# Performance work log

Measured on AMD Instinct MI355X. Metric: run time of the kernel, lower is better.

Reference implementation:

```python
import jax, jax.numpy as jnp
import numpy as np

N_NODES = 50000
N_EDGES = 800000
NUM_FEATS = 512
NUM_CLASSES = 64
NUM_LAYERS = 4


def setup_inputs() -> dict:
    key = jax.random.key(0)
    k1, k2, k3 = jax.random.split(key, 3)
    x = jax.random.normal(k1, (N_NODES, NUM_FEATS), dtype=jnp.float32)
    # glorot init for weight [num_feats, num_classes]
    scale = jnp.sqrt(6.0 / (NUM_FEATS + NUM_CLASSES)).astype(jnp.float32)
    weight = jax.random.uniform(k2, (NUM_FEATS, NUM_CLASSES), dtype=jnp.float32,
                                minval=-scale, maxval=scale)
    edge_index = jax.random.randint(k3, (2, N_EDGES), 0, N_NODES, dtype=jnp.int64)
    return {"x": x, "weight": weight, "edge_index": edge_index}


def reference(x, weight, edge_index):
    row, col = edge_index[0], edge_index[1]  # [E], [E]
    # symmetric GCN normalization: deg^{-1/2}[row] * deg^{-1/2}[col]
    deg = jax.ops.segment_sum(jnp.ones((edge_index.shape[1],), dtype=x.dtype),
                              row, num_segments=x.shape[0])  # [N]
    deg_inv_sqrt = jnp.where(deg > 0, jax.lax.rsqrt(jnp.maximum(deg, 1e-12)), 0.0)
    norm = (deg_inv_sqrt[row] * deg_inv_sqrt[col])[:, None]  # [E, 1]

    h = x @ weight  # [N, num_classes] (dropout skipped: eval mode)
    for _ in range(NUM_LAYERS):
        # gather source features, scale by edge norm, scatter-add to destinations
        msg = norm * h[row]  # [E, num_classes]
        h = jax.ops.segment_sum(msg, col, num_segments=x.shape[0])  # [N, num_classes]
        # type_norm == 'None' -> layers_bn is identity
    return h
```

## Files before the change

### kernel.cpp

```cpp
#include <hip/hip_runtime.h>
#include <hip/hip_fp16.h>

#define NFEAT 512
#define NCLS  64
#define NNODES 50000
#define NW    (NNODES / 4)
#define NB    256
#define NG    8
#define SLOTS 64

typedef unsigned int uint;
using short8 = __attribute__((ext_vector_type(8))) short;
using f32x4  = __attribute__((ext_vector_type(4))) float;

static __device__ __forceinline__ unsigned short f32_to_bf16_rne(float f) {
    unsigned u = __float_as_uint(f);
    unsigned r = u + 0x7FFFu + ((u >> 16) & 1u);
    return (unsigned short)(r >> 16);
}
static __device__ __forceinline__ float bf16_to_f32(unsigned short b) {
    return __uint_as_float(((unsigned)b) << 16);
}
static __device__ __forceinline__ uint cvt_pk_bf16(float a, float b) {
    uint r;
    asm("v_cvt_pk_bf16_f32 %0, %1, %2" : "=v"(r) : "v"(a), "v"(b));
    return r;
}
static __device__ __forceinline__ void split_bf16x8(const float* xs, short8& ahi, short8& alo) {
    union { uint u[4]; short8 s; } H, L;
#pragma unroll
    for (int t = 0; t < 4; ++t) {
        float x0 = xs[2 * t], x1 = xs[2 * t + 1];
        uint hp = cvt_pk_bf16(x0, x1);
        float f0 = __uint_as_float(hp << 16);
        float f1 = __uint_as_float(hp & 0xffff0000u);
        uint lp = cvt_pk_bf16(x0 - f0, x1 - f1);
        H.u[t] = hp; L.u[t] = lp;
    }
    ahi = H.s; alo = L.s;
}


__global__ __launch_bounds__(256) void hist_packw_kernel(
        const int* __restrict__ row, const int* __restrict__ col,
        const float* __restrict__ w,
        uint* __restrict__ degB, uint* __restrict__ cntB,
        short8* __restrict__ wp, int E, int CH) {
    __shared__ __align__(16) uint h[2 * NW];
    int b = blockIdx.x;
    if (b < NB) {
        for (int i = threadIdx.x; i < 2 * NW; i += 256) h[i] = 0;
        __syncthreads();
        int e0 = b * CH, e1 = min(E, e0 + CH);
        for (int e = e0 + threadIdx.x; e < e1; e += 256) {
            int c = col[e], r = row[e];
            atomicAdd(&h[c >> 2], 1u << ((c & 3) * 8));
            atomicAdd(&h[NW + (r >> 2)], 1u << ((r & 3) * 8));
        }
        __syncthreads();
        uint4* cb = reinterpret_cast<uint4*>(cntB + (size_t)b * NW);
        uint4* db = reinterpret_cast<uint4*>(degB + (size_t)b * NW);
        const uint4* c4 = reinterpret_cast<const uint4*>(h);
        const uint4* d4 = reinterpret_cast<const uint4*>(h + NW);
        for (int i = threadIdx.x; i < NW / 4; i += 256) cb[i] = c4[i];
        for (int i = threadIdx.x; i < NW / 4; i += 256) db[i] = d4[i];
        return;
    }
    int gid = (b - NB) * 256 + threadIdx.x;
    int lane = gid & 63;
    int F = gid >> 6;
    int s = F & 1;
    int nt = (F >> 1) & 3;
    int kk = F >> 3;
    int k0 = kk * 32 + (lane >> 4) * 8;
    int c  = nt * 16 + (lane & 15);
    short8 v;
#pragma unroll
    for (int j = 0; j < 8; ++j) {
        float xv = w[(k0 + j) * NCLS + c];
        unsigned short hi = f32_to_bf16_rne(xv);
        unsigned short outv = hi;
        if (s) outv = f32_to_bf16_rne(xv - bf16_to_f32(hi));
        v[j] = (short)outv;
    }
    wp[gid] = v;
}


__global__ __launch_bounds__(256) void scan_sub_kernel(uint* __restrict__ cntB,
                                                       const uint* __restrict__ degB,
                                                       uint* __restrict__ cntSub,
                                                       uint* __restrict__ degSub) {
    int gid = blockIdx.x * 256 + threadIdx.x;
    if (gid >= 2 * NG * NW) return;
    int half = gid / (NG * NW);
    int rem  = gid % (NG * NW);
    int g = rem / NW, wi = rem % NW;
    if (half == 0) {
        uint run = 0;
#pragma unroll 8
        for (int b = g * 32; b < g * 32 + 32; ++b) {
            uint v = cntB[(size_t)b * NW + wi];
            cntB[(size_t)b * NW + wi] = run;
            run += v;
        }
        cntSub[(size_t)g * NW + wi] = run;
    } else {
        uint run = 0;
#pragma unroll 8
        for (int b = g * 32; b < g * 32 + 32; ++b) run += degB[(size_t)b * NW + wi];
        degSub[(size_t)g * NW + wi] = run;
    }
}


__global__ __launch_bounds__(256) void scan_top_kernel(uint* __restrict__ cntSub,
                                                       const uint* __restrict__ degSub,
                                                       int* __restrict__ cntTot,
                                                       float* __restrict__ dinv) {
    int wi = blockIdx.x * 256 + threadIdx.x;
    if (wi >= NW) return;
    uint run = 0;
#pragma unroll
    for (int g = 0; g < NG; ++g) {
        uint v = cntSub[(size_t)g * NW + wi];
        cntSub[(size_t)g * NW + wi] = run;
        run += v;
    }
    int4 t = { (int)(run & 255), (int)((run >> 8) & 255),
               (int)((run >> 16) & 255), (int)(run >> 24) };
    *reinterpret_cast<int4*>(cntTot + wi * 4) = t;

    uint run2 = 0;
#pragma unroll
    for (int g = 0; g < NG; ++g) run2 += degSub[(size_t)g * NW + wi];
    int d0 = run2 & 255, d1 = (run2 >> 8) & 255, d2 = (run2 >> 16) & 255, d3 = run2 >> 24;
    float4 dv;
    dv.x = d0 ? rsqrtf((float)d0) : 0.0f;
    dv.y = d1 ? rsqrtf((float)d1) : 0.0f;
    dv.z = d2 ? rsqrtf((float)d2) : 0.0f;
    dv.w = d3 ? rsqrtf((float)d3) : 0.0f;
    *reinterpret_cast<float4*>(dinv + wi * 4) = dv;
}


__global__ __launch_bounds__(256, 2) void place_matmul_kernel(
        const int* __restrict__ row, const int* __restrict__ col,
        const uint* __restrict__ offB, const uint* __restrict__ cntSub,
        int* __restrict__ slots,
        const float* __restrict__ x, const short8* __restrict__ wp,
        const float* __restrict__ dinv, __half* __restrict__ u0,
        int N, int E, int CH) {
    __shared__ __align__(16) uint sh[NW];
    int b = blockIdx.x;

    if (b < NB) {
        uint4* c4 = reinterpret_cast<uint4*>(sh);
        const uint4* o4 = reinterpret_cast<const uint4*>(offB + (size_t)b * NW);
        const uint4* s4 = reinterpret_cast<const uint4*>(cntSub + (size_t)(b >> 5) * NW);
        for (int i = threadIdx.x; i < NW / 4; i += 256) {
            uint4 a = o4[i], d = s4[i];
            a.x += d.x; a.y += d.y; a.z += d.z; a.w += d.w;
            c4[i] = a;
        }
        __syncthreads();
        int e0 = b * CH, e1 = min(E, e0 + CH);
        for (int e = e0 + threadIdx.x; e < e1; e += 256) {
            int c = col[e];
            uint old = atomicAdd(&sh[c >> 2], 1u << ((c & 3) * 8));
            int pos = (old >> ((c & 3) * 8)) & 255;
            if (pos < SLOTS) slots[(c << 6) + pos] = row[e];
        }
        return;
    }

    int tile = b - NB;
    int tid = threadIdx.x;
    int wave = tid >> 6, lane = tid & 63;
    int rlo = lane & 15, khi = lane >> 4;
    int row0 = tile * 128 + wave * 32;

    size_t roff[2];
#pragma unroll
    for (int rg = 0; rg < 2; ++rg) {
        int rr = row0 + rg * 16 + rlo;
        if (rr > N - 1) rr = N - 1;
        roff[rg] = (size_t)rr * NFEAT + khi * 8;
    }

    f32x4 acc[2][4];
#pragma unroll
    for (int rg = 0; rg < 2; ++rg)
#pragma unroll
        for (int nt = 0; nt < 4; ++nt) acc[rg][nt] = f32x4{0.f, 0.f, 0.f, 0.f};

    const short8* fbase = wp + lane;
    for (int ch = 0; ch < 4; ++ch) {
#pragma unroll
        for (int kk = 0; kk < 4; ++kk) {
            const short8* fb = fbase + ch * 2048 + kk * 512;
            short8 bh0 = fb[0],   bl0 = fb[64];
            short8 bh1 = fb[128], bl1 = fb[192];
            short8 bh2 = fb[256], bl2 = fb[320];
            short8 bh3 = fb[384], bl3 = fb[448];
            int kg = ch * 128 + kk * 32;
#pragma unroll
            for (int rg = 0; rg < 2; ++rg) {
                float4 xa = *reinterpret_cast<const float4*>(x + roff[rg] + kg);
                float4 xb = *reinterpret_cast<const float4*>(x + roff[rg] + kg + 4);
                float xs[8] = {xa.x, xa.y, xa.z, xa.w, xb.x, xb.y, xb.z, xb.w};
                short8 ahi, alo;
                split_bf16x8(xs, ahi, alo);
                acc[rg][0] = __builtin_amdgcn_mfma_f32_16x16x32_bf16(ahi, bh0, acc[rg][0], 0, 0, 0);
                acc[rg][1] = __builtin_amdgcn_mfma_f32_16x16x32_bf16(ahi, bh1, acc[rg][1], 0, 0, 0);
                acc[rg][2] = __builtin_amdgcn_mfma_f32_16x16x32_bf16(ahi, bh2, acc[rg][2], 0, 0, 0);
                acc[rg][3] = __builtin_amdgcn_mfma_f32_16x16x32_bf16(ahi, bh3, acc[rg][3], 0, 0, 0);
                acc[rg][0] = __builtin_amdgcn_mfma_f32_16x16x32_bf16(alo, bh0, acc[rg][0], 0, 0, 0);
                acc[rg][1] = __builtin_amdgcn_mfma_f32_16x16x32_bf16(alo, bh1, acc[rg][1], 0, 0, 0);
                acc[rg][2] = __builtin_amdgcn_mfma_f32_16x16x32_bf16(alo, bh2, acc[rg][2], 0, 0, 0);
                acc[rg][3] = __builtin_amdgcn_mfma_f32_16x16x32_bf16(alo, bh3, acc[rg][3], 0, 0, 0);
                acc[rg][0] = __builtin_amdgcn_mfma_f32_16x16x32_bf16(ahi, bl0, acc[rg][0], 0, 0, 0);
                acc[rg][1] = __builtin_amdgcn_mfma_f32_16x16x32_bf16(ahi, bl1, acc[rg][1], 0, 0, 0);
                acc[rg][2] = __builtin_amdgcn_mfma_f32_16x16x32_bf16(ahi, bl2, acc[rg][2], 0, 0, 0);
                acc[rg][3] = __builtin_amdgcn_mfma_f32_16x16x32_bf16(ahi, bl3, acc[rg][3], 0, 0, 0);
            }
        }
    }

#pragma unroll
    for (int rg = 0; rg < 2; ++rg) {
        int rbase = row0 + rg * 16 + khi * 4;
#pragma unroll
        for (int j = 0; j < 4; ++j) {
            int r = rbase + j;
            if (r < N) {
                float dn = dinv[r];
                __half* op = u0 + ((size_t)r << 6) + rlo;
                op[0]  = __float2half(acc[rg][0][j] * dn);
                op[16] = __float2half(acc[rg][1][j] * dn);
                op[32] = __float2half(acc[rg][2][j] * dn);
                op[48] = __float2half(acc[rg][3][j] * dn);
            }
        }
    }
}


__global__ __launch_bounds__(256) void gather_kernel(const __half* __restrict__ u,
                                                     const int* __restrict__ cntTot,
                                                     int* __restrict__ slots,
                                                     const float* __restrict__ dinv,
                                                     __half* __restrict__ out_h,
                                                     float* __restrict__ out_f,
                                                     int N, int sq, int dosort) {
    int wid = blockIdx.x * 4 + (threadIdx.x >> 6);
    if (wid >= N) return;
    int lane = threadIdx.x & 63;
    int q = lane >> 3;
    int p = lane & 7;
    int cq = cntTot[wid];
    cq = (cq < SLOTS) ? cq : SLOTS;
    int* sl = slots + (wid << 6);
    int s_l = sl[lane];

    if (dosort) {
        int v = (lane < cq) ? s_l : 0x7fffffff;
#pragma unroll
        for (int k = 2; k <= 64; k <<= 1) {
#pragma unroll
            for (int j = k >> 1; j >= 1; j >>= 1) {
                int pv = __shfl_xor(v, j);
                int lo = min(v, pv), hi = max(v, pv);
                bool up = ((lane & k) == 0);
                v = (((lane & j) == 0) == up) ? lo : hi;
            }
        }
        s_l = v;
        if (lane < cq) sl[lane] = v;
    }

    float a0=0.f,a1=0.f,a2=0.f,a3=0.f,a4=0.f,a5=0.f,a6=0.f,a7=0.f;
    float b0=0.f,b1=0.f,b2=0.f,b3=0.f,b4=0.f,b5=0.f,b6=0.f,b7=0.f;
#pragma unroll
    for (int j = 0; j < 8; j += 2) {
        int i0 = q + 8 * j;
        int i1 = q + 8 * (j + 1);
        int s0 = __shfl(s_l, i0);
        int s1 = __shfl(s_l, i1);
        if (i0 < cq) {
            uint4 d0 = *reinterpret_cast<const uint4*>(u + ((size_t)s0 << 6) + p * 8);
            float2 f0 = __half22float2(*reinterpret_cast<__half2*>(&d0.x));
            float2 f1 = __half22float2(*reinterpret_cast<__half2*>(&d0.y));
            float2 f2 = __half22float2(*reinterpret_cast<__half2*>(&d0.z));
            float2 f3 = __half22float2(*reinterpret_cast<__half2*>(&d0.w));
            a0 += f0.x; a1 += f0.y; a2 += f1.x; a3 += f1.y;
            a4 += f2.x; a5 += f2.y; a6 += f3.x; a7 += f3.y;
        }
        if (i1 < cq) {
            uint4 d1 = *reinterpret_cast<const uint4*>(u + ((size_t)s1 << 6) + p * 8);
            float2 g0 = __half22float2(*reinterpret_cast<__half2*>(&d1.x));
            float2 g1 = __half22float2(*reinterpret_cast<__half2*>(&d1.y));
            float2 g2 = __half22float2(*reinterpret_cast<__half2*>(&d1.z));
            float2 g3 = __half22float2(*reinterpret_cast<__half2*>(&d1.w));
            b0 += g0.x; b1 += g0.y; b2 += g1.x; b3 += g1.y;
            b4 += g2.x; b5 += g2.y; b6 += g3.x; b7 += g3.y;
        }
    }
    a0 += b0; a1 += b1; a2 += b2; a3 += b3;
    a4 += b4; a5 += b5; a6 += b6; a7 += b7;
#pragma unroll
    for (int off = 8; off < 64; off <<= 1) {
        a0 += __shfl_xor(a0, off); a1 += __shfl_xor(a1, off);
        a2 += __shfl_xor(a2, off); a3 += __shfl_xor(a3, off);
        a4 += __shfl_xor(a4, off); a5 += __shfl_xor(a5, off);
        a6 += __shfl_xor(a6, off); a7 += __shfl_xor(a7, off);
    }
    if (q == 0) {
        float sc = dinv[wid];
        if (sq) {
            sc *= sc;
            __half2 h0 = __floats2half2_rn(a0 * sc, a1 * sc);
            __half2 h1 = __floats2half2_rn(a2 * sc, a3 * sc);
            __half2 h2 = __floats2half2_rn(a4 * sc, a5 * sc);
            __half2 h3 = __floats2half2_rn(a6 * sc, a7 * sc);
            uint4 d;
            d.x = *reinterpret_cast<uint*>(&h0);
            d.y = *reinterpret_cast<uint*>(&h1);
            d.z = *reinterpret_cast<uint*>(&h2);
            d.w = *reinterpret_cast<uint*>(&h3);
            *reinterpret_cast<uint4*>(out_h + ((size_t)wid << 6) + p * 8) = d;
        } else {
            float4 r0 = {a0 * sc, a1 * sc, a2 * sc, a3 * sc};
            float4 r1 = {a4 * sc, a5 * sc, a6 * sc, a7 * sc};
            float4* op = reinterpret_cast<float4*>(out_f + ((size_t)wid << 6) + p * 8);
            op[0] = r0;
            op[1] = r1;
        }
    }
}


extern "C" void kernel_launch(void* const* d_in, const int* in_sizes, int n_in,
                              void* d_out, int out_size, void* d_ws, size_t ws_size,
                              hipStream_t stream) {
    const float* x = (const float*)d_in[0];
    const float* w = (const float*)d_in[1];
    const int*   ei = (const int*)d_in[2];

    int N = in_sizes[0] / NFEAT;
    int E = in_sizes[2] / 2;
    const int* row = ei;
    const int* col = ei + E;
    float* out = (float*)d_out;

    auto align256 = [](size_t v) { return (v + 255) & ~(size_t)255; };
    char* ws = (char*)d_ws;
    size_t off = 0;
    uint* cntB   = (uint*)(ws + off);   off += align256((size_t)NB * NW * sizeof(uint));
    uint* degB   = (uint*)(ws + off);   off += align256((size_t)NB * NW * sizeof(uint));
    uint* cntSub = (uint*)(ws + off);   off += align256((size_t)NG * NW * sizeof(uint));
    uint* degSub = (uint*)(ws + off);   off += align256((size_t)NG * NW * sizeof(uint));
    int* cntTot  = (int*)(ws + off);    off += align256((size_t)NNODES * sizeof(int));
    float* dinv  = (float*)(ws + off);  off += align256((size_t)NNODES * sizeof(float));
    short8* wp   = (short8*)(ws + off); off += align256((size_t)8192 * sizeof(short8));
    int* slots   = (int*)(ws + off);    off += align256((size_t)NNODES * SLOTS * sizeof(int));
    __half* uA   = (__half*)(ws + off); off += align256((size_t)NNODES * NCLS * sizeof(__half));
    __half* uB   = (__half*)(ws + off); off += align256((size_t)NNODES * NCLS * sizeof(__half));

    int CH = (E + NB - 1) / NB;

    hist_packw_kernel<<<NB + 32, 256, 0, stream>>>(row, col, w, degB, cntB, wp, E, CH);
    scan_sub_kernel<<<(2 * NG * NW + 255) / 256, 256, 0, stream>>>(cntB, degB, cntSub, degSub);
    scan_top_kernel<<<(NW + 255) / 256, 256, 0, stream>>>(cntSub, degSub, cntTot, dinv);
    int nmm = (N + 127) / 128;
    place_matmul_kernel<<<NB + nmm, 256, 0, stream>>>(row, col, cntB, cntSub, slots,
                                                      x, wp, dinv, uA, N, E, CH);

    int ngrid = (N + 3) / 4;
    gather_kernel<<<ngrid, 256, 0, stream>>>(uA, cntTot, slots, dinv, uB, nullptr, N, 1, 1);
    gather_kernel<<<ngrid, 256, 0, stream>>>(uB, cntTot, slots, dinv, uA, nullptr, N, 1, 0);
    gather_kernel<<<ngrid, 256, 0, stream>>>(uA, cntTot, slots, dinv, uB, nullptr, N, 1, 0);
    gather_kernel<<<ngrid, 256, 0, stream>>>(uB, cntTot, slots, dinv, nullptr, out, N, 0, 0);
}
```

Before: 160.6 us.

## Store slot indices as 16-bit and use compact 4-bit LDS rank counters

```diff
diff --git a/kernel.cpp b/kernel.cpp
--- a/kernel.cpp
+++ b/kernel.cpp
@@ -5,11 +5,13 @@
 #define NCLS  64
 #define NNODES 50000
 #define NW    (NNODES / 4)
+#define NW8   (NNODES / 8)
 #define NB    256
 #define NG    8
 #define SLOTS 64
 
 typedef unsigned int uint;
+typedef unsigned short ushort;
 using short8 = __attribute__((ext_vector_type(8))) short;
 using f32x4  = __attribute__((ext_vector_type(4))) float;
 
@@ -144,32 +146,31 @@
 }
 
 
-__global__ __launch_bounds__(256, 2) void place_matmul_kernel(
+__global__ __launch_bounds__(256, 4) void place_matmul_kernel(
         const int* __restrict__ row, const int* __restrict__ col,
         const uint* __restrict__ offB, const uint* __restrict__ cntSub,
-        int* __restrict__ slots,
+        ushort* __restrict__ slots,
         const float* __restrict__ x, const short8* __restrict__ wp,
         const float* __restrict__ dinv, __half* __restrict__ u0,
         int N, int E, int CH) {
-    __shared__ __align__(16) uint sh[NW];
+    __shared__ __align__(16) uint sh[NW8];
     int b = blockIdx.x;
 
     if (b < NB) {
-        uint4* c4 = reinterpret_cast<uint4*>(sh);
-        const uint4* o4 = reinterpret_cast<const uint4*>(offB + (size_t)b * NW);
-        const uint4* s4 = reinterpret_cast<const uint4*>(cntSub + (size_t)(b >> 5) * NW);
-        for (int i = threadIdx.x; i < NW / 4; i += 256) {
-            uint4 a = o4[i], d = s4[i];
-            a.x += d.x; a.y += d.y; a.z += d.z; a.w += d.w;
-            c4[i] = a;
-        }
+        for (int i = threadIdx.x; i < NW8; i += 256) sh[i] = 0;
         __syncthreads();
+        const uint* ob = offB + (size_t)b * NW;
+        const uint* sb = cntSub + (size_t)(b >> 5) * NW;
         int e0 = b * CH, e1 = min(E, e0 + CH);
         for (int e = e0 + threadIdx.x; e < e1; e += 256) {
             int c = col[e];
-            uint old = atomicAdd(&sh[c >> 2], 1u << ((c & 3) * 8));
-            int pos = (old >> ((c & 3) * 8)) & 255;
-            if (pos < SLOTS) slots[(c << 6) + pos] = row[e];
+            int r = row[e];
+            uint old = atomicAdd(&sh[c >> 3], 1u << ((c & 7) * 4));
+            int rank = (old >> ((c & 7) * 4)) & 15;
+            int sh8 = (c & 3) * 8;
+            int base = (int)((ob[c >> 2] >> sh8) & 255) + (int)((sb[c >> 2] >> sh8) & 255);
+            int pos = base + rank;
+            if (pos < SLOTS) slots[(c << 6) + pos] = (ushort)r;
         }
         return;
     }
@@ -248,7 +249,7 @@
 
 __global__ __launch_bounds__(256) void gather_kernel(const __half* __restrict__ u,
                                                      const int* __restrict__ cntTot,
-                                                     int* __restrict__ slots,
+                                                     ushort* __restrict__ slots,
                                                      const float* __restrict__ dinv,
                                                      __half* __restrict__ out_h,
                                                      float* __restrict__ out_f,
@@ -260,11 +261,11 @@
     int p = lane & 7;
     int cq = cntTot[wid];
     cq = (cq < SLOTS) ? cq : SLOTS;
-    int* sl = slots + (wid << 6);
+    ushort* sl = slots + (wid << 6);
     int s_l = sl[lane];
 
     if (dosort) {
-        int v = (lane < cq) ? s_l : 0x7fffffff;
+        int v = (lane < cq) ? s_l : 0xFFFF;
 #pragma unroll
         for (int k = 2; k <= 64; k <<= 1) {
 #pragma unroll
@@ -276,7 +277,7 @@
             }
         }
         s_l = v;
-        if (lane < cq) sl[lane] = v;
+        if (lane < cq) sl[lane] = (ushort)v;
     }
 
     float a0=0.f,a1=0.f,a2=0.f,a3=0.f,a4=0.f,a5=0.f,a6=0.f,a7=0.f;
@@ -363,7 +364,7 @@
     int* cntTot  = (int*)(ws + off);    off += align256((size_t)NNODES * sizeof(int));
     float* dinv  = (float*)(ws + off);  off += align256((size_t)NNODES * sizeof(float));
     short8* wp   = (short8*)(ws + off); off += align256((size_t)8192 * sizeof(short8));
-    int* slots   = (int*)(ws + off);    off += align256((size_t)NNODES * SLOTS * sizeof(int));
+    ushort* slots = (ushort*)(ws + off); off += align256((size_t)NNODES * SLOTS * sizeof(ushort));
     __half* uA   = (__half*)(ws + off); off += align256((size_t)NNODES * NCLS * sizeof(__half));
     __half* uB   = (__half*)(ws + off); off += align256((size_t)NNODES * NCLS * sizeof(__half));
 
```

New measurement: 167.3 us. +4.2%, slower.

## Store neighbor slots as 16-bit indices and gather two nodes per wave

Applied to the files above, without the earlier changes.

```diff
diff --git a/kernel.cpp b/kernel.cpp
--- a/kernel.cpp
+++ b/kernel.cpp
@@ -10,6 +10,7 @@
 #define SLOTS 64
 
 typedef unsigned int uint;
+typedef unsigned short ushort;
 using short8 = __attribute__((ext_vector_type(8))) short;
 using f32x4  = __attribute__((ext_vector_type(4))) float;
 
@@ -147,7 +148,7 @@
 __global__ __launch_bounds__(256, 2) void place_matmul_kernel(
         const int* __restrict__ row, const int* __restrict__ col,
         const uint* __restrict__ offB, const uint* __restrict__ cntSub,
-        int* __restrict__ slots,
+        ushort* __restrict__ slots,
         const float* __restrict__ x, const short8* __restrict__ wp,
         const float* __restrict__ dinv, __half* __restrict__ u0,
         int N, int E, int CH) {
@@ -169,7 +170,8 @@
             int c = col[e];
             uint old = atomicAdd(&sh[c >> 2], 1u << ((c & 3) * 8));
             int pos = (old >> ((c & 3) * 8)) & 255;
-            if (pos < SLOTS) slots[(c << 6) + pos] = row[e];
+            if (pos < SLOTS)
+                __builtin_nontemporal_store((ushort)row[e], &slots[(c << 6) + pos]);
         }
         return;
     }
@@ -248,93 +250,107 @@
 
 __global__ __launch_bounds__(256) void gather_kernel(const __half* __restrict__ u,
                                                      const int* __restrict__ cntTot,
-                                                     int* __restrict__ slots,
+                                                     ushort* __restrict__ slots,
                                                      const float* __restrict__ dinv,
                                                      __half* __restrict__ out_h,
                                                      float* __restrict__ out_f,
                                                      int N, int sq, int dosort) {
-    int wid = blockIdx.x * 4 + (threadIdx.x >> 6);
-    if (wid >= N) return;
-    int lane = threadIdx.x & 63;
+    int wave = threadIdx.x >> 6, lane = threadIdx.x & 63;
     int q = lane >> 3;
     int p = lane & 7;
-    int cq = cntTot[wid];
-    cq = (cq < SLOTS) ? cq : SLOTS;
-    int* sl = slots + (wid << 6);
-    int s_l = sl[lane];
+    int wbase = blockIdx.x * 8 + wave * 2;
+    if (wbase >= N) return;
+
+    int sv[2], cqv[2];
+    float acc[2][8];
+#pragma unroll
+    for (int nn = 0; nn < 2; ++nn) {
+        int wid = wbase + nn;
+        sv[nn] = 0xFFFF; cqv[nn] = 0;
+        if (wid < N) {
+            int cq = cntTot[wid];
+            cqv[nn] = (cq < SLOTS) ? cq : SLOTS;
+            sv[nn] = slots[((size_t)wid << 6) + lane];
+        }
+#pragma unroll
+        for (int t = 0; t < 8; ++t) acc[nn][t] = 0.f;
+    }
 
     if (dosort) {
-        int v = (lane < cq) ? s_l : 0x7fffffff;
-#pragma unroll
-        for (int k = 2; k <= 64; k <<= 1) {
-#pragma unroll
-            for (int j = k >> 1; j >= 1; j >>= 1) {
-                int pv = __shfl_xor(v, j);
-                int lo = min(v, pv), hi = max(v, pv);
-                bool up = ((lane & k) == 0);
-                v = (((lane & j) == 0) == up) ? lo : hi;
+#pragma unroll
+        for (int nn = 0; nn < 2; ++nn) {
+            int wid = wbase + nn;
+            if (wid >= N) continue;
+            int v = (lane < cqv[nn]) ? sv[nn] : 0xFFFF;
+#pragma unroll
+            for (int k = 2; k <= 64; k <<= 1) {
+#pragma unroll
+                for (int j = k >> 1; j >= 1; j >>= 1) {
+                    int pv = __shfl_xor(v, j);
+                    int lo = min(v, pv), hi = max(v, pv);
+                    bool up = ((lane & k) == 0);
+                    v = (((lane & j) == 0) == up) ? lo : hi;
+                }
             }
-        }
-        s_l = v;
-        if (lane < cq) sl[lane] = v;
-    }
-
-    float a0=0.f,a1=0.f,a2=0.f,a3=0.f,a4=0.f,a5=0.f,a6=0.f,a7=0.f;
-    float b0=0.f,b1=0.f,b2=0.f,b3=0.f,b4=0.f,b5=0.f,b6=0.f,b7=0.f;
-#pragma unroll
-    for (int j = 0; j < 8; j += 2) {
-        int i0 = q + 8 * j;
-        int i1 = q + 8 * (j + 1);
-        int s0 = __shfl(s_l, i0);
-        int s1 = __shfl(s_l, i1);
-        if (i0 < cq) {
-            uint4 d0 = *reinterpret_cast<const uint4*>(u + ((size_t)s0 << 6) + p * 8);
-            float2 f0 = __half22float2(*reinterpret_cast<__half2*>(&d0.x));
-            float2 f1 = __half22float2(*reinterpret_cast<__half2*>(&d0.y));
-            float2 f2 = __half22float2(*reinterpret_cast<__half2*>(&d0.z));
-            float2 f3 = __half22float2(*reinterpret_cast<__half2*>(&d0.w));
-            a0 += f0.x; a1 += f0.y; a2 += f1.x; a3 += f1.y;
-            a4 += f2.x; a5 += f2.y; a6 += f3.x; a7 += f3.y;
-        }
-        if (i1 < cq) {
-            uint4 d1 = *reinterpret_cast<const uint4*>(u + ((size_t)s1 << 6) + p * 8);
-            float2 g0 = __half22float2(*reinterpret_cast<__half2*>(&d1.x));
-            float2 g1 = __half22float2(*reinterpret_cast<__half2*>(&d1.y));
-            float2 g2 = __half22float2(*reinterpret_cast<__half2*>(&d1.z));
-            float2 g3 = __half22float2(*reinterpret_cast<__half2*>(&d1.w));
-            b0 += g0.x; b1 += g0.y; b2 += g1.x; b3 += g1.y;
-            b4 += g2.x; b5 += g2.y; b6 += g3.x; b7 += g3.y;
-        }
-    }
-    a0 += b0; a1 += b1; a2 += b2; a3 += b3;
-    a4 += b4; a5 += b5; a6 += b6; a7 += b7;
+            sv[nn] = v;
+            if (lane < cqv[nn]) slots[((size_t)wid << 6) + lane] = (ushort)v;
+        }
+    }
+
+#pragma unroll
+    for (int j = 0; j < 8; ++j) {
+        int idx = q + 8 * j;
+#pragma unroll
+        for (int nn = 0; nn < 2; ++nn) {
+            int s = __shfl(sv[nn], idx);
+            if (idx < cqv[nn]) {
+                uint4 d = *reinterpret_cast<const uint4*>(u + ((size_t)s << 6) + p * 8);
+                float2 f0 = __half22float2(*reinterpret_cast<__half2*>(&d.x));
+                float2 f1 = __half22float2(*reinterpret_cast<__half2*>(&d.y));
+                float2 f2 = __half22float2(*reinterpret_cast<__half2*>(&d.z));
+                float2 f3 = __half22float2(*reinterpret_cast<__half2*>(&d.w));
+                acc[nn][0] += f0.x; acc[nn][1] += f0.y;
+                acc[nn][2] += f1.x; acc[nn][3] += f1.y;
+                acc[nn][4] += f2.x; acc[nn][5] += f2.y;
+                acc[nn][6] += f3.x; acc[nn][7] += f3.y;
+            }
+        }
+    }
+
 #pragma unroll
     for (int off = 8; off < 64; off <<= 1) {
-        a0 += __shfl_xor(a0, off); a1 += __shfl_xor(a1, off);
-        a2 += __shfl_xor(a2, off); a3 += __shfl_xor(a3, off);
-        a4 += __shfl_xor(a4, off); a5 += __shfl_xor(a5, off);
-        a6 += __shfl_xor(a6, off); a7 += __shfl_xor(a7, off);
-    }
+#pragma unroll
+        for (int nn = 0; nn < 2; ++nn)
+#pragma unroll
+            for (int t = 0; t < 8; ++t)
+                acc[nn][t] += __shfl_xor(acc[nn][t], off);
+    }
+
     if (q == 0) {
-        float sc = dinv[wid];
-        if (sq) {
-            sc *= sc;
-            __half2 h0 = __floats2half2_rn(a0 * sc, a1 * sc);
-            __half2 h1 = __floats2half2_rn(a2 * sc, a3 * sc);
-            __half2 h2 = __floats2half2_rn(a4 * sc, a5 * sc);
-            __half2 h3 = __floats2half2_rn(a6 * sc, a7 * sc);
-            uint4 d;
-            d.x = *reinterpret_cast<uint*>(&h0);
-            d.y = *reinterpret_cast<uint*>(&h1);
-            d.z = *reinterpret_cast<uint*>(&h2);
-            d.w = *reinterpret_cast<uint*>(&h3);
-            *reinterpret_cast<uint4*>(out_h + ((size_t)wid << 6) + p * 8) = d;
-        } else {
-            float4 r0 = {a0 * sc, a1 * sc, a2 * sc, a3 * sc};
-            float4 r1 = {a4 * sc, a5 * sc, a6 * sc, a7 * sc};
-            float4* op = reinterpret_cast<float4*>(out_f + ((size_t)wid << 6) + p * 8);
-            op[0] = r0;
-            op[1] = r1;
+#pragma unroll
+        for (int nn = 0; nn < 2; ++nn) {
+            int wid = wbase + nn;
+            if (wid >= N) continue;
+            float sc = dinv[wid];
+            if (sq) {
+                float s2 = sc * sc;
+                __half2 h0 = __floats2half2_rn(acc[nn][0] * s2, acc[nn][1] * s2);
+                __half2 h1 = __floats2half2_rn(acc[nn][2] * s2, acc[nn][3] * s2);
+                __half2 h2 = __floats2half2_rn(acc[nn][4] * s2, acc[nn][5] * s2);
+                __half2 h3 = __floats2half2_rn(acc[nn][6] * s2, acc[nn][7] * s2);
+                uint4 d;
+                d.x = *reinterpret_cast<uint*>(&h0);
+                d.y = *reinterpret_cast<uint*>(&h1);
+                d.z = *reinterpret_cast<uint*>(&h2);
+                d.w = *reinterpret_cast<uint*>(&h3);
+                *reinterpret_cast<uint4*>(out_h + ((size_t)wid << 6) + p * 8) = d;
+            } else {
+                float4 r0 = {acc[nn][0] * sc, acc[nn][1] * sc, acc[nn][2] * sc, acc[nn][3] * sc};
+                float4 r1 = {acc[nn][4] * sc, acc[nn][5] * sc, acc[nn][6] * sc, acc[nn][7] * sc};
+                float4* op = reinterpret_cast<float4*>(out_f + ((size_t)wid << 6) + p * 8);
+                op[0] = r0;
+                op[1] = r1;
+            }
         }
     }
 }
@@ -363,7 +379,7 @@
     int* cntTot  = (int*)(ws + off);    off += align256((size_t)NNODES * sizeof(int));
     float* dinv  = (float*)(ws + off);  off += align256((size_t)NNODES * sizeof(float));
     short8* wp   = (short8*)(ws + off); off += align256((size_t)8192 * sizeof(short8));
-    int* slots   = (int*)(ws + off);    off += align256((size_t)NNODES * SLOTS * sizeof(int));
+    ushort* slots = (ushort*)(ws + off); off += align256((size_t)NNODES * SLOTS * sizeof(ushort));
     __half* uA   = (__half*)(ws + off); off += align256((size_t)NNODES * NCLS * sizeof(__half));
     __half* uB   = (__half*)(ws + off); off += align256((size_t)NNODES * NCLS * sizeof(__half));
 
@@ -376,7 +392,7 @@
     place_matmul_kernel<<<NB + nmm, 256, 0, stream>>>(row, col, cntB, cntSub, slots,
                                                       x, wp, dinv, uA, N, E, CH);
 
-    int ngrid = (N + 3) / 4;
+    int ngrid = (N + 7) / 8;
     gather_kernel<<<ngrid, 256, 0, stream>>>(uA, cntTot, slots, dinv, uB, nullptr, N, 1, 1);
     gather_kernel<<<ngrid, 256, 0, stream>>>(uB, cntTot, slots, dinv, uA, nullptr, N, 1, 0);
     gather_kernel<<<ngrid, 256, 0, stream>>>(uA, cntTot, slots, dinv, uB, nullptr, N, 1, 0);
```

Measured after the change: 166.4 us. 1.04x slower.
